# Kernel optimization log

Hardware: AMD Instinct MI355X
Metric: run time of the kernel (lower is better)

## Reference

```python
import jax, jax.numpy as jnp
import numpy as np

HIDDEN = 256
Q_HIDDEN = 1024
FILTER = 31
WINDOW = 1024


def setup_inputs() -> dict:
    key = jax.random.key(0)
    ks = jax.random.split(key, 10)
    T, B, H, Q = 4096, 64, HIDDEN, Q_HIDDEN
    tokens = jax.random.normal(ks[0], (T, B, H), dtype=jnp.float32)
    tokens_mask = jnp.ones((B, T), dtype=bool)
    num_tokens = jax.random.randint(ks[1], (B,), 0, T)
    query = jax.random.normal(ks[2], (1, B, Q), dtype=jnp.float32)
    cumulative_alignment = jax.random.uniform(ks[3], (B, T), dtype=jnp.float32)
    initial_cumulative_alignment = jax.random.uniform(ks[4], (B, 1), dtype=jnp.float32)
    window_start = jax.random.randint(ks[5], (B,), 0, T - WINDOW)
    # parameters
    conv_w = jax.random.normal(ks[6], (H, 1, FILTER), dtype=jnp.float32) * (1.0 / np.sqrt(FILTER))
    conv_b = jnp.zeros((H,), dtype=jnp.float32)
    wq = jax.random.normal(ks[7], (H, Q), dtype=jnp.float32) * (1.0 / np.sqrt(Q))
    bq = jnp.zeros((H,), dtype=jnp.float32)
    ws = jax.random.normal(ks[8], (H,), dtype=jnp.float32) * (1.0 / np.sqrt(H))
    return {
        'tokens': tokens, 'tokens_mask': tokens_mask, 'num_tokens': num_tokens,
        'query': query, 'cumulative_alignment': cumulative_alignment,
        'initial_cumulative_alignment': initial_cumulative_alignment,
        'window_start': window_start, 'conv_w': conv_w, 'conv_b': conv_b,
        'wq': wq, 'bq': bq, 'ws': ws,
    }


def reference(tokens, tokens_mask, num_tokens, query, cumulative_alignment,
              initial_cumulative_alignment, window_start, conv_w, conv_b, wq, bq, ws):
    T, B, H = tokens.shape
    K = conv_w.shape[-1]
    pad = (K - 1) // 2
    WL = min(WINDOW, T)

    # zero cumulative alignment at padding positions
    ca = jnp.where(tokens_mask, cumulative_alignment, 0.0)  # [B, T]
    # left-pad with initial_cumulative_alignment, right-pad with zeros
    init = jnp.broadcast_to(initial_cumulative_alignment[:, :, None], (B, 1, pad))
    loc = jnp.concatenate([init, ca[:, None, :], jnp.zeros((B, 1, pad), jnp.float32)], axis=-1)  # [B,1,T+2p]

    # dynamic per-batch windows
    win = jnp.arange(WL)
    idx_t = win[:, None] + window_start[None, :]                     # [WL, B]
    tokens_w = jnp.take_along_axis(tokens, idx_t[:, :, None], axis=0)  # [WL, B, H]
    idx_m = win[None, :] + window_start[:, None]                     # [B, WL]
    mask_w = jnp.take_along_axis(tokens_mask, idx_m, axis=1)         # [B, WL]
    idx_l = jnp.arange(WL + 2 * pad)[None, :] + window_start[:, None]  # [B, WL+2p]
    loc_w = jnp.take_along_axis(loc, idx_l[:, None, :], axis=2)     # [B, 1, WL+2p]

    # conv1d over cumulative alignment window -> [B, H, WL]
    conv = jax.lax.conv_general_dilated(loc_w, conv_w, (1,), 'VALID',
                                        dimension_numbers=('NCH', 'OIH', 'NCH'))
    conv = conv + conv_b[None, :, None]

    q = query[0] @ wq.T + bq                                         # [B, H]
    feat = jnp.tanh(conv + q[:, :, None])                            # [B, H, WL]
    score = jnp.einsum('bhw,h->bw', feat, ws)                        # [B, WL]
    score = jnp.where(mask_w, score, -jnp.inf)
    alignment = jax.nn.softmax(score, axis=1)                        # [B, WL]

    context = jnp.einsum('bw,wbh->bh', alignment, tokens_w)          # [B, H]

    # scatter window alignment back to full length
    alignment_full = jnp.zeros((B, T), jnp.float32).at[jnp.arange(B)[:, None], idx_m].add(alignment)

    new_ws = jnp.argmax(alignment_full, axis=1) - WL // 2
    new_ws = jnp.clip(jnp.minimum(new_ws, num_tokens - WL), 0)

    cum = ca + alignment_full
    return context, cum, alignment_full, new_ws
```

## Files before the change

### kernel.cpp

```cpp
#include <hip/hip_runtime.h>
#include <math.h>

#define T_LEN 4096
#define B_N 64
#define H_N 256
#define Q_N 1024
#define K_F 31
#define PAD 15
#define WL 1024

__device__ __forceinline__ float tanh_fast(float x) {
    float e = __expf(2.0f * x);
    return 1.0f - 2.0f / (e + 1.0f);
}

__global__ __launch_bounds__(256) void k_score(
        const float* __restrict__ query, const float* __restrict__ wq,
        const float* __restrict__ bq, const float* __restrict__ conv_b,
        const float* __restrict__ ca, const int* __restrict__ mask,
        const float* __restrict__ init, const int* __restrict__ wstart,
        const float* __restrict__ conv_w, const float* __restrict__ ws_vec,
        float* __restrict__ scoreP) {
    int hc = blockIdx.x, b = blockIdx.y, tid = threadIdx.x;
    int h0 = hc * 32;
    __shared__ __align__(16) float qbuf[Q_N];
    __shared__ __align__(16) float loc[1056];
    __shared__ __align__(16) float cw[32][32];
    __shared__ float qv[32], wv[32];
    int wsb = wstart[b];

    for (int i = tid; i < Q_N; i += 256) qbuf[i] = query[b * Q_N + i];
    for (int i = tid; i < 1056; i += 256) {
        float v = 0.f;
        if (i < 1054) {
            int p = wsb + i;
            if (p < PAD) v = init[b];
            else {
                int t = p - PAD;
                if (t < T_LEN && mask[b * T_LEN + t] != 0) v = ca[b * T_LEN + t];
            }
        }
        loc[i] = v;
    }
    for (int i = tid; i < 32 * 32; i += 256) {
        int r = i >> 5, c = i & 31;
        cw[r][c] = (c < K_F) ? conv_w[(h0 + r) * K_F + c] : 0.f;
    }
    if (tid < 32) wv[tid] = ws_vec[h0 + tid];
    __syncthreads();

    {
        int h = tid >> 3, part = tid & 7;
        const float4* wrow = (const float4*)(wq + (size_t)(h0 + h) * Q_N) + part * 32;
        const float4* qrow = (const float4*)qbuf + part * 32;
        float acc = 0.f;
        #pragma unroll 8
        for (int i = 0; i < 32; i++) {
            float4 a = wrow[i], c = qrow[i];
            acc += a.x * c.x + a.y * c.y + a.z * c.z + a.w * c.w;
        }
        acc += __shfl_xor(acc, 1);
        acc += __shfl_xor(acc, 2);
        acc += __shfl_xor(acc, 4);
        if (part == 0) qv[h] = acc + bq[h0 + h] + conv_b[h0 + h];
    }
    __syncthreads();

    int w0 = tid * 4;
    float l[35];
    #pragma unroll
    for (int j = 0; j < 35; j++) l[j] = loc[w0 + j];

    float s0 = 0.f, s1 = 0.f, s2 = 0.f, s3 = 0.f;
    for (int hh = 0; hh < 32; hh++) {
        float bias = qv[hh];
        float c0 = bias, c1 = bias, c2 = bias, c3 = bias;
        #pragma unroll
        for (int k = 0; k < 32; k += 4) {
            float4 cq = *(const float4*)&cw[hh][k];
            c0 += l[k + 0] * cq.x; c1 += l[k + 1] * cq.x; c2 += l[k + 2] * cq.x; c3 += l[k + 3] * cq.x;
            c0 += l[k + 1] * cq.y; c1 += l[k + 2] * cq.y; c2 += l[k + 3] * cq.y; c3 += l[k + 4] * cq.y;
            c0 += l[k + 2] * cq.z; c1 += l[k + 3] * cq.z; c2 += l[k + 4] * cq.z; c3 += l[k + 5] * cq.z;
            c0 += l[k + 3] * cq.w; c1 += l[k + 4] * cq.w; c2 += l[k + 5] * cq.w; c3 += l[k + 6] * cq.w;
        }
        float wh = wv[hh];
        s0 += wh * tanh_fast(c0); s1 += wh * tanh_fast(c1);
        s2 += wh * tanh_fast(c2); s3 += wh * tanh_fast(c3);
    }
    *(float4*)&scoreP[((size_t)hc * B_N + b) * WL + w0] = make_float4(s0, s1, s2, s3);
}

__global__ __launch_bounds__(256) void k_softmax(
        const float* __restrict__ scoreP, const int* __restrict__ mask,
        const float* __restrict__ ca, const int* __restrict__ wstart,
        const int* __restrict__ num_tokens, float* __restrict__ alignW,
        float* __restrict__ out_ctx, float* __restrict__ out_cum,
        float* __restrict__ out_align, float* __restrict__ out_nws) {
    int b = blockIdx.x, tid = threadIdx.x;
    __shared__ float sc[WL];
    __shared__ float red[256];
    __shared__ int redi[256];
    int wsb = wstart[b];
    for (int w = tid; w < WL; w += 256) {
        float s = 0.f;
        #pragma unroll
        for (int p = 0; p < 8; p++) s += scoreP[((size_t)p * B_N + b) * WL + w];
        if (mask[b * T_LEN + wsb + w] == 0) s = -3.0e38f;
        sc[w] = s;
    }
    __syncthreads();
    float mx = -3.0e38f;
    for (int w = tid; w < WL; w += 256) mx = fmaxf(mx, sc[w]);
    red[tid] = mx; __syncthreads();
    for (int s = 128; s > 0; s >>= 1) {
        if (tid < s) red[tid] = fmaxf(red[tid], red[tid + s]);
        __syncthreads();
    }
    mx = red[0]; __syncthreads();
    float lsum = 0.f;
    for (int w = tid; w < WL; w += 256) {
        float e = __expf(sc[w] - mx);
        sc[w] = e; lsum += e;
    }
    red[tid] = lsum; __syncthreads();
    for (int s = 128; s > 0; s >>= 1) {
        if (tid < s) red[tid] += red[tid + s];
        __syncthreads();
    }
    float inv = 1.0f / red[0];
    __syncthreads();
    float bv = -1.f; int bi = 0;
    for (int w = tid; w < WL; w += 256) {
        float a = sc[w] * inv;
        sc[w] = a;
        alignW[b * WL + w] = a;
        if (a > bv) { bv = a; bi = w; }
    }
    red[tid] = bv; redi[tid] = bi; __syncthreads();
    for (int s = 128; s > 0; s >>= 1) {
        if (tid < s) {
            float ov = red[tid + s]; int oi = redi[tid + s];
            if (ov > red[tid] || (ov == red[tid] && oi < redi[tid])) { red[tid] = ov; redi[tid] = oi; }
        }
        __syncthreads();
    }
    if (tid == 0) {
        int tstar = wsb + redi[0];
        int nws = tstar - WL / 2;
        int lim = num_tokens[b] - WL;
        nws = nws < lim ? nws : lim;
        nws = nws > 0 ? nws : 0;
        out_nws[b] = (float)nws;
    }
    const int4* m4p = (const int4*)(mask + (size_t)b * T_LEN);
    const float4* c4p = (const float4*)(ca + (size_t)b * T_LEN);
    float4* oa4 = (float4*)(out_align + (size_t)b * T_LEN);
    float4* oc4 = (float4*)(out_cum + (size_t)b * T_LEN);
    for (int t4 = tid; t4 < T_LEN / 4; t4 += 256) {
        int t = t4 * 4;
        int4 m4 = m4p[t4];
        float4 c4 = c4p[t4];
        float4 av, cum;
        int j0 = t - wsb;
        av.x = (j0 >= 0 && j0 < WL) ? sc[j0] : 0.f;
        av.y = (j0 + 1 >= 0 && j0 + 1 < WL) ? sc[j0 + 1] : 0.f;
        av.z = (j0 + 2 >= 0 && j0 + 2 < WL) ? sc[j0 + 2] : 0.f;
        av.w = (j0 + 3 >= 0 && j0 + 3 < WL) ? sc[j0 + 3] : 0.f;
        cum.x = (m4.x != 0 ? c4.x : 0.f) + av.x;
        cum.y = (m4.y != 0 ? c4.y : 0.f) + av.y;
        cum.z = (m4.z != 0 ? c4.z : 0.f) + av.z;
        cum.w = (m4.w != 0 ? c4.w : 0.f) + av.w;
        oa4[t4] = av;
        oc4[t4] = cum;
    }
    out_ctx[b * H_N + tid] = 0.f;
}

__global__ __launch_bounds__(256) void k_context(
        const float* __restrict__ tokens, const float* __restrict__ alignW,
        const int* __restrict__ wstart, float* __restrict__ out_ctx) {
    int wc = blockIdx.x, b = blockIdx.y, tid = threadIdx.x;
    __shared__ float av[64];
    __shared__ __align__(16) float4 red4[256];
    if (tid < 64) av[tid] = alignW[b * WL + wc * 64 + tid];
    __syncthreads();
    int h4 = (tid & 63) * 4, wj = tid >> 6;
    int wsb = wstart[b];
    const float* tokbase = tokens + ((size_t)(wsb + wc * 64 + wj) * B_N + b) * H_N + h4;
    float4 acc = make_float4(0.f, 0.f, 0.f, 0.f);
    #pragma unroll 4
    for (int j = 0; j < 16; j++) {
        float a = av[wj + 4 * j];
        float4 t4 = *(const float4*)(tokbase + (size_t)(4 * j) * B_N * H_N);
        acc.x += a * t4.x; acc.y += a * t4.y; acc.z += a * t4.z; acc.w += a * t4.w;
    }
    red4[tid] = acc;
    __syncthreads();
    if (tid < 64) {
        float4 r0 = red4[tid], r1 = red4[tid + 64], r2 = red4[tid + 128], r3 = red4[tid + 192];
        float* dst = &out_ctx[b * H_N + tid * 4];
        atomicAdd(dst + 0, r0.x + r1.x + r2.x + r3.x);
        atomicAdd(dst + 1, r0.y + r1.y + r2.y + r3.y);
        atomicAdd(dst + 2, r0.z + r1.z + r2.z + r3.z);
        atomicAdd(dst + 3, r0.w + r1.w + r2.w + r3.w);
    }
}

extern "C" void kernel_launch(void* const* d_in, const int* in_sizes, int n_in,
                              void* d_out, int out_size, void* d_ws, size_t ws_size,
                              hipStream_t stream) {
    const float* tokens     = (const float*)d_in[0];
    const int*   mask       = (const int*)  d_in[1];
    const int*   num_tokens = (const int*)  d_in[2];
    const float* query      = (const float*)d_in[3];
    const float* ca         = (const float*)d_in[4];
    const float* init       = (const float*)d_in[5];
    const int*   wstart     = (const int*)  d_in[6];
    const float* conv_w     = (const float*)d_in[7];
    const float* conv_b     = (const float*)d_in[8];
    const float* wq         = (const float*)d_in[9];
    const float* bq         = (const float*)d_in[10];
    const float* ws_vec     = (const float*)d_in[11];

    float* out       = (float*)d_out;
    float* out_ctx   = out;
    float* out_cum   = out + 16384;
    float* out_align = out + 16384 + 262144;
    float* out_nws   = out + 16384 + 2 * 262144;

    float* scoreP = (float*)d_ws;
    float* alignW = scoreP + 8 * B_N * WL;

    k_score  <<<dim3(8, B_N),   dim3(256), 0, stream>>>(query, wq, bq, conv_b, ca, mask, init,
                                                        wstart, conv_w, ws_vec, scoreP);
    k_softmax<<<dim3(B_N),      dim3(256), 0, stream>>>(scoreP, mask, ca, wstart, num_tokens, alignW,
                                                        out_ctx, out_cum, out_align, out_nws);
    k_context<<<dim3(16, B_N),  dim3(256), 0, stream>>>(tokens, alignW, wstart, out_ctx);
}
```

Measured before the change: 377.2 us.

## Move full-length scatter into context kernel and use wave-shuffle softmax reductions

```diff
diff --git a/kernel.cpp b/kernel.cpp
--- a/kernel.cpp
+++ b/kernel.cpp
@@ -67,9 +67,10 @@
     __syncthreads();
 
     int w0 = tid * 4;
-    float l[35];
-    #pragma unroll
-    for (int j = 0; j < 35; j++) l[j] = loc[w0 + j];
+    float4 lv4[9];
+    #pragma unroll
+    for (int j = 0; j < 9; j++) lv4[j] = *(const float4*)&loc[w0 + 4 * j];
+    const float* l = (const float*)lv4;
 
     float s0 = 0.f, s1 = 0.f, s2 = 0.f, s3 = 0.f;
     for (int hh = 0; hh < 32; hh++) {
@@ -92,117 +93,119 @@
 
 __global__ __launch_bounds__(256) void k_softmax(
         const float* __restrict__ scoreP, const int* __restrict__ mask,
-        const float* __restrict__ ca, const int* __restrict__ wstart,
-        const int* __restrict__ num_tokens, float* __restrict__ alignW,
-        float* __restrict__ out_ctx, float* __restrict__ out_cum,
-        float* __restrict__ out_align, float* __restrict__ out_nws) {
+        const int* __restrict__ wstart, const int* __restrict__ num_tokens,
+        float* __restrict__ alignW, float* __restrict__ out_ctx,
+        float* __restrict__ out_nws) {
     int b = blockIdx.x, tid = threadIdx.x;
-    __shared__ float sc[WL];
-    __shared__ float red[256];
-    __shared__ int redi[256];
+    __shared__ float red[8];
+    __shared__ float redv[4];
+    __shared__ int redi[4];
     int wsb = wstart[b];
-    for (int w = tid; w < WL; w += 256) {
-        float s = 0.f;
-        #pragma unroll
-        for (int p = 0; p < 8; p++) s += scoreP[((size_t)p * B_N + b) * WL + w];
-        if (mask[b * T_LEN + wsb + w] == 0) s = -3.0e38f;
-        sc[w] = s;
-    }
-    __syncthreads();
-    float mx = -3.0e38f;
-    for (int w = tid; w < WL; w += 256) mx = fmaxf(mx, sc[w]);
-    red[tid] = mx; __syncthreads();
-    for (int s = 128; s > 0; s >>= 1) {
-        if (tid < s) red[tid] = fmaxf(red[tid], red[tid + s]);
-        __syncthreads();
-    }
-    mx = red[0]; __syncthreads();
+
+    float s[4];
+    #pragma unroll
+    for (int k = 0; k < 4; k++) {
+        int w = tid + 256 * k;
+        float v = 0.f;
+        #pragma unroll
+        for (int p = 0; p < 8; p++) v += scoreP[((size_t)p * B_N + b) * WL + w];
+        if (mask[b * T_LEN + wsb + w] == 0) v = -3.0e38f;
+        s[k] = v;
+    }
+    float mx = fmaxf(fmaxf(s[0], s[1]), fmaxf(s[2], s[3]));
+    #pragma unroll
+    for (int o = 32; o > 0; o >>= 1) mx = fmaxf(mx, __shfl_xor(mx, o));
+    if ((tid & 63) == 0) red[tid >> 6] = mx;
+    __syncthreads();
+    mx = fmaxf(fmaxf(red[0], red[1]), fmaxf(red[2], red[3]));
+
     float lsum = 0.f;
-    for (int w = tid; w < WL; w += 256) {
-        float e = __expf(sc[w] - mx);
-        sc[w] = e; lsum += e;
-    }
-    red[tid] = lsum; __syncthreads();
-    for (int s = 128; s > 0; s >>= 1) {
-        if (tid < s) red[tid] += red[tid + s];
-        __syncthreads();
-    }
-    float inv = 1.0f / red[0];
-    __syncthreads();
+    #pragma unroll
+    for (int k = 0; k < 4; k++) { s[k] = __expf(s[k] - mx); lsum += s[k]; }
+    #pragma unroll
+    for (int o = 32; o > 0; o >>= 1) lsum += __shfl_xor(lsum, o);
+    if ((tid & 63) == 0) red[4 + (tid >> 6)] = lsum;
+    __syncthreads();
+    float inv = 1.0f / (red[4] + red[5] + red[6] + red[7]);
+
     float bv = -1.f; int bi = 0;
-    for (int w = tid; w < WL; w += 256) {
-        float a = sc[w] * inv;
-        sc[w] = a;
-        alignW[b * WL + w] = a;
-        if (a > bv) { bv = a; bi = w; }
-    }
-    red[tid] = bv; redi[tid] = bi; __syncthreads();
-    for (int s = 128; s > 0; s >>= 1) {
-        if (tid < s) {
-            float ov = red[tid + s]; int oi = redi[tid + s];
-            if (ov > red[tid] || (ov == red[tid] && oi < redi[tid])) { red[tid] = ov; redi[tid] = oi; }
-        }
-        __syncthreads();
-    }
+    #pragma unroll
+    for (int k = 0; k < 4; k++) {
+        float a = s[k] * inv;
+        alignW[b * WL + tid + 256 * k] = a;
+        if (a > bv) { bv = a; bi = tid + 256 * k; }
+    }
+    #pragma unroll
+    for (int o = 32; o > 0; o >>= 1) {
+        float ov = __shfl_xor(bv, o); int oi = __shfl_xor(bi, o);
+        if (ov > bv || (ov == bv && oi < bi)) { bv = ov; bi = oi; }
+    }
+    if ((tid & 63) == 0) { redv[tid >> 6] = bv; redi[tid >> 6] = bi; }
+    __syncthreads();
     if (tid == 0) {
-        int tstar = wsb + redi[0];
+        float v = redv[0]; int i = redi[0];
+        #pragma unroll
+        for (int k = 1; k < 4; k++)
+            if (redv[k] > v || (redv[k] == v && redi[k] < i)) { v = redv[k]; i = redi[k]; }
+        int tstar = wsb + i;
         int nws = tstar - WL / 2;
         int lim = num_tokens[b] - WL;
         nws = nws < lim ? nws : lim;
         nws = nws > 0 ? nws : 0;
         out_nws[b] = (float)nws;
     }
-    const int4* m4p = (const int4*)(mask + (size_t)b * T_LEN);
-    const float4* c4p = (const float4*)(ca + (size_t)b * T_LEN);
-    float4* oa4 = (float4*)(out_align + (size_t)b * T_LEN);
-    float4* oc4 = (float4*)(out_cum + (size_t)b * T_LEN);
-    for (int t4 = tid; t4 < T_LEN / 4; t4 += 256) {
-        int t = t4 * 4;
-        int4 m4 = m4p[t4];
-        float4 c4 = c4p[t4];
-        float4 av, cum;
-        int j0 = t - wsb;
-        av.x = (j0 >= 0 && j0 < WL) ? sc[j0] : 0.f;
-        av.y = (j0 + 1 >= 0 && j0 + 1 < WL) ? sc[j0 + 1] : 0.f;
-        av.z = (j0 + 2 >= 0 && j0 + 2 < WL) ? sc[j0 + 2] : 0.f;
-        av.w = (j0 + 3 >= 0 && j0 + 3 < WL) ? sc[j0 + 3] : 0.f;
-        cum.x = (m4.x != 0 ? c4.x : 0.f) + av.x;
-        cum.y = (m4.y != 0 ? c4.y : 0.f) + av.y;
-        cum.z = (m4.z != 0 ? c4.z : 0.f) + av.z;
-        cum.w = (m4.w != 0 ? c4.w : 0.f) + av.w;
-        oa4[t4] = av;
-        oc4[t4] = cum;
-    }
     out_ctx[b * H_N + tid] = 0.f;
 }
 
-__global__ __launch_bounds__(256) void k_context(
+__global__ __launch_bounds__(256) void k_ctx_scatter(
         const float* __restrict__ tokens, const float* __restrict__ alignW,
-        const int* __restrict__ wstart, float* __restrict__ out_ctx) {
-    int wc = blockIdx.x, b = blockIdx.y, tid = threadIdx.x;
+        const int* __restrict__ mask, const float* __restrict__ ca,
+        const int* __restrict__ wstart, float* __restrict__ out_ctx,
+        float* __restrict__ out_align, float* __restrict__ out_cum) {
+    int bx = blockIdx.x, b = blockIdx.y, tid = threadIdx.x;
+    int wsb = wstart[b];
     __shared__ float av[64];
     __shared__ __align__(16) float4 red4[256];
-    if (tid < 64) av[tid] = alignW[b * WL + wc * 64 + tid];
-    __syncthreads();
-    int h4 = (tid & 63) * 4, wj = tid >> 6;
-    int wsb = wstart[b];
-    const float* tokbase = tokens + ((size_t)(wsb + wc * 64 + wj) * B_N + b) * H_N + h4;
-    float4 acc = make_float4(0.f, 0.f, 0.f, 0.f);
-    #pragma unroll 4
-    for (int j = 0; j < 16; j++) {
-        float a = av[wj + 4 * j];
-        float4 t4 = *(const float4*)(tokbase + (size_t)(4 * j) * B_N * H_N);
-        acc.x += a * t4.x; acc.y += a * t4.y; acc.z += a * t4.z; acc.w += a * t4.w;
-    }
-    red4[tid] = acc;
-    __syncthreads();
-    if (tid < 64) {
-        float4 r0 = red4[tid], r1 = red4[tid + 64], r2 = red4[tid + 128], r3 = red4[tid + 192];
-        float* dst = &out_ctx[b * H_N + tid * 4];
-        atomicAdd(dst + 0, r0.x + r1.x + r2.x + r3.x);
-        atomicAdd(dst + 1, r0.y + r1.y + r2.y + r3.y);
-        atomicAdd(dst + 2, r0.z + r1.z + r2.z + r3.z);
-        atomicAdd(dst + 3, r0.w + r1.w + r2.w + r3.w);
+    if (bx < 16) {
+        if (tid < 64) av[tid] = alignW[b * WL + bx * 64 + tid];
+        __syncthreads();
+        int h4 = (tid & 63) * 4, wj = tid >> 6;
+        const float* tokbase = tokens + ((size_t)(wsb + bx * 64 + wj) * B_N + b) * H_N + h4;
+        float4 acc = make_float4(0.f, 0.f, 0.f, 0.f);
+        #pragma unroll
+        for (int j = 0; j < 16; j++) {
+            float a = av[wj + 4 * j];
+            float4 t4 = *(const float4*)(tokbase + (size_t)(4 * j) * B_N * H_N);
+            acc.x += a * t4.x; acc.y += a * t4.y; acc.z += a * t4.z; acc.w += a * t4.w;
+        }
+        red4[tid] = acc;
+        __syncthreads();
+        if (tid < 64) {
+            float4 r0 = red4[tid], r1 = red4[tid + 64], r2 = red4[tid + 128], r3 = red4[tid + 192];
+            float* dst = &out_ctx[b * H_N + tid * 4];
+            atomicAdd(dst + 0, r0.x + r1.x + r2.x + r3.x);
+            atomicAdd(dst + 1, r0.y + r1.y + r2.y + r3.y);
+            atomicAdd(dst + 2, r0.z + r1.z + r2.z + r3.z);
+            atomicAdd(dst + 3, r0.w + r1.w + r2.w + r3.w);
+        }
+    } else {
+        int t4 = (bx - 16) * 256 + tid;
+        int4 m4 = ((const int4*)(mask + (size_t)b * T_LEN))[t4];
+        float4 c4 = ((const float4*)(ca + (size_t)b * T_LEN))[t4];
+        const float* aw = alignW + (size_t)b * WL;
+        int j0 = t4 * 4 - wsb;
+        float4 av4;
+        av4.x = ((unsigned)(j0 + 0) < WL) ? aw[j0 + 0] : 0.f;
+        av4.y = ((unsigned)(j0 + 1) < WL) ? aw[j0 + 1] : 0.f;
+        av4.z = ((unsigned)(j0 + 2) < WL) ? aw[j0 + 2] : 0.f;
+        av4.w = ((unsigned)(j0 + 3) < WL) ? aw[j0 + 3] : 0.f;
+        float4 cum;
+        cum.x = (m4.x != 0 ? c4.x : 0.f) + av4.x;
+        cum.y = (m4.y != 0 ? c4.y : 0.f) + av4.y;
+        cum.z = (m4.z != 0 ? c4.z : 0.f) + av4.z;
+        cum.w = (m4.w != 0 ? c4.w : 0.f) + av4.w;
+        ((float4*)(out_align + (size_t)b * T_LEN))[t4] = av4;
+        ((float4*)(out_cum + (size_t)b * T_LEN))[t4] = cum;
     }
 }
 
@@ -231,9 +234,10 @@
     float* scoreP = (float*)d_ws;
     float* alignW = scoreP + 8 * B_N * WL;
 
-    k_score  <<<dim3(8, B_N),   dim3(256), 0, stream>>>(query, wq, bq, conv_b, ca, mask, init,
-                                                        wstart, conv_w, ws_vec, scoreP);
-    k_softmax<<<dim3(B_N),      dim3(256), 0, stream>>>(scoreP, mask, ca, wstart, num_tokens, alignW,
-                                                        out_ctx, out_cum, out_align, out_nws);
-    k_context<<<dim3(16, B_N),  dim3(256), 0, stream>>>(tokens, alignW, wstart, out_ctx);
-}
+    k_score      <<<dim3(8, B_N),  dim3(256), 0, stream>>>(query, wq, bq, conv_b, ca, mask, init,
+                                                           wstart, conv_w, ws_vec, scoreP);
+    k_softmax    <<<dim3(B_N),     dim3(256), 0, stream>>>(scoreP, mask, wstart, num_tokens,
+                                                           alignW, out_ctx, out_nws);
+    k_ctx_scatter<<<dim3(20, B_N), dim3(256), 0, stream>>>(tokens, alignW, mask, ca, wstart,
+                                                           out_ctx, out_align, out_cum);
+}
```

Result: no change. 372.5 us (-1.2%).
